# Performance work log

Hardware: AMD Instinct MI355X
Metric: run time of the kernel (lower is better)

The kernel has to match this reference:

```python
import jax, jax.numpy as jnp
import numpy as np

B, S, H = 32, 128, 768
MH, MT = 6, 8            # max holder / target span sizes
M = max(MH, MT)          # max span size -> M conv widths (1..M)
KH, KT = 4, 4            # max n holders / targets per sentence


def _forward(embedding, mask, wh, bh, wt, bt, wi, bi, we, be):
    Bz, Sz, Hz = embedding.shape
    # --- multi-scale span averaging (Conv1d with identity box filters == moving mean) ---
    cs = jnp.concatenate([jnp.zeros((Bz, 1, Hz), embedding.dtype),
                          jnp.cumsum(embedding, axis=1)], axis=1)  # [B,S+1,H]
    reps = [embedding]
    for w in range(2, M + 1):
        mean = (cs[:, w:, :] - cs[:, :-w, :]) / float(w)          # [B,S-w+1,H]
        reps.append(jnp.pad(mean, ((0, 0), (0, w - 1), (0, 0))))  # zero-pad tail like torch.cat
    span = jnp.concatenate(reps, axis=1)                          # [B, M*S, H]; index = S*width_idx + start
    # --- span validity masks (span must fit within sentence length) ---
    lengths = jnp.sum(mask, axis=1)                               # [B]
    pos = jnp.arange(Sz)
    widths = jnp.arange(M)
    base = pos[None, None, :] < (lengths[:, None, None] - widths[None, :, None])  # [B,M,S]
    holder_valid = (base & (widths[None, :, None] < MH)).reshape(Bz, M * Sz)
    target_valid = (base & (widths[None, :, None] < MT)).reshape(Bz, M * Sz)
    # --- span scoring (sigmoid linear), invalid spans forced to -1 ---
    hs = jnp.where(holder_valid, jax.nn.sigmoid(span @ wh + bh), -1.0)  # [B, M*S]
    ts = jnp.where(target_valid, jax.nn.sigmoid(span @ wt + bt), -1.0)
    # --- top-k span selection (== argsort descending, take first K) ---
    vt, it = jax.lax.top_k(ts, KT)
    vh, ih = jax.lax.top_k(hs, KH)
    tval = vt > 0.0                                                # [B,KT]
    hval = vh > 0.0                                                # [B,KH]
    trep = jnp.take_along_axis(span, it[:, :, None], axis=1)      # [B,KT,H]
    hrep = jnp.take_along_axis(span, ih[:, :, None], axis=1)      # [B,KH,H]
    implicit_input = trep * tval[:, :, None].astype(span.dtype)   # zeros where invalid
    pair_valid = (hval[:, :, None] & tval[:, None, :])            # [B,KH,KT]
    pair = jnp.concatenate([jnp.broadcast_to(hrep[:, :, None, :], (Bz, KH, KT, Hz)),
                            jnp.broadcast_to(trep[:, None, :, :], (Bz, KH, KT, Hz))], axis=-1)
    explicit_input = (pair * pair_valid[..., None].astype(span.dtype)).reshape(Bz, KH * KT, 2 * Hz)
    implicit_logits = implicit_input @ wi + bi                    # [B,KT,4]
    explicit_logits = explicit_input @ we + be                    # [B,KH*KT,4]
    return implicit_logits, explicit_logits, hs, ts


def setup_inputs() -> dict:
    key = jax.random.key(0)
    ks = jax.random.split(key, 8)
    embedding = jax.random.normal(ks[0], (B, S, H), jnp.float32)
    mask = jax.random.randint(ks[1], (B, S), 0, 2).astype(jnp.int32)
    wh = jax.random.normal(ks[2], (H,), jnp.float32) * 0.02
    bh = jnp.zeros((), jnp.float32)
    wt = jax.random.normal(ks[3], (H,), jnp.float32) * 0.02
    bt = jnp.zeros((), jnp.float32)
    wi = jax.random.normal(ks[4], (H, 4), jnp.float32) * 0.02
    bi = jnp.zeros((4,), jnp.float32)
    we = jax.random.normal(ks[5], (2 * H, 4), jnp.float32) * 0.02
    be = jnp.zeros((4,), jnp.float32)
    return dict(embedding=embedding, mask=mask, wh=wh, bh=bh, wt=wt, bt=bt,
                wi=wi, bi=bi, we=we, be=be)


def reference(embedding, mask, wh, bh, wt, bt, wi, bi, we, be):
    return _forward(embedding, mask, wh, bh, wt, bt, wi, bi, we, be)
```

## Files before the change

### kernel.cpp

```cpp
#include <hip/hip_runtime.h>

namespace {
constexpr int Bsz = 32;
constexpr int Ssz = 128;
constexpr int Hsz = 768;
constexpr int Msz = 8;
constexpr int MHs = 6;
constexpr int NSPAN = Msz * Ssz;
}

__device__ __forceinline__ bool gtpair(float av, int ai, float bv, int bi) {
    return (av > bv) || (av == bv && ai < bi);
}

struct Top4 { float v[4]; int ix[4]; };

__device__ __forceinline__ void t4_init(Top4& t) {
#pragma unroll
    for (int k = 0; k < 4; ++k) { t.v[k] = -3.f; t.ix[k] = 0x7fffffff; }
}

__device__ __forceinline__ void t4_insert_g(Top4& a, float cv, int ci) {
    bool g0 = gtpair(cv, ci, a.v[0], a.ix[0]);
    bool g1 = gtpair(cv, ci, a.v[1], a.ix[1]);
    bool g2 = gtpair(cv, ci, a.v[2], a.ix[2]);
    bool g3 = gtpair(cv, ci, a.v[3], a.ix[3]);
    float nv3 = g2 ? a.v[2]  : (g3 ? cv : a.v[3]);
    int   ni3 = g2 ? a.ix[2] : (g3 ? ci : a.ix[3]);
    float nv2 = g1 ? a.v[1]  : (g2 ? cv : a.v[2]);
    int   ni2 = g1 ? a.ix[1] : (g2 ? ci : a.ix[2]);
    float nv1 = g0 ? a.v[0]  : (g1 ? cv : a.v[1]);
    int   ni1 = g0 ? a.ix[0] : (g1 ? ci : a.ix[1]);
    float nv0 = g0 ? cv : a.v[0];
    int   ni0 = g0 ? ci : a.ix[0];
    a.v[0] = nv0; a.ix[0] = ni0;
    a.v[1] = nv1; a.ix[1] = ni1;
    a.v[2] = nv2; a.ix[2] = ni2;
    a.v[3] = nv3; a.ix[3] = ni3;
}

__device__ __forceinline__ void t4_merge_into(Top4& a, const Top4& b) {
#pragma unroll
    for (int k = 0; k < 4; ++k) t4_insert_g(a, b.v[k], b.ix[k]);
}

__device__ __forceinline__ Top4 t4_wave_merge(Top4 t) {
#pragma unroll
    for (int off = 1; off < 64; off <<= 1) {
        Top4 o;
#pragma unroll
        for (int k = 0; k < 4; ++k) {
            o.v[k]  = __shfl_xor(t.v[k], off);
            o.ix[k] = __shfl_xor(t.ix[k], off);
        }
        t4_merge_into(t, o);
    }
    return t;
}

__global__ __launch_bounds__(256) void row_dots_kernel(
    const float* __restrict__ emb, const float* __restrict__ wh,
    const float* __restrict__ wt, float* __restrict__ dh, float* __restrict__ dt)
{
    int wave = blockIdx.x * 4 + (threadIdx.x >> 6);
    int lane = threadIdx.x & 63;
    int row0 = wave * 2;

    const float4* wh4 = (const float4*)wh;
    const float4* wt4 = (const float4*)wt;
    float4 WH0 = wh4[lane], WH1 = wh4[lane + 64], WH2 = wh4[lane + 128];
    float4 WT0 = wt4[lane], WT1 = wt4[lane + 64], WT2 = wt4[lane + 128];

    const float4* r0 = (const float4*)(emb + (size_t)row0 * Hsz);
    const float4* r1 = r0 + (Hsz / 4);
    float4 a0 = r0[lane], a1 = r0[lane + 64], a2 = r0[lane + 128];
    float4 b0 = r1[lane], b1 = r1[lane + 64], b2 = r1[lane + 128];

    float ph0 = 0.f, pt0 = 0.f, ph1 = 0.f, pt1 = 0.f;
    ph0 = fmaf(a0.x, WH0.x, fmaf(a0.y, WH0.y, fmaf(a0.z, WH0.z, fmaf(a0.w, WH0.w, ph0))));
    ph0 = fmaf(a1.x, WH1.x, fmaf(a1.y, WH1.y, fmaf(a1.z, WH1.z, fmaf(a1.w, WH1.w, ph0))));
    ph0 = fmaf(a2.x, WH2.x, fmaf(a2.y, WH2.y, fmaf(a2.z, WH2.z, fmaf(a2.w, WH2.w, ph0))));
    pt0 = fmaf(a0.x, WT0.x, fmaf(a0.y, WT0.y, fmaf(a0.z, WT0.z, fmaf(a0.w, WT0.w, pt0))));
    pt0 = fmaf(a1.x, WT1.x, fmaf(a1.y, WT1.y, fmaf(a1.z, WT1.z, fmaf(a1.w, WT1.w, pt0))));
    pt0 = fmaf(a2.x, WT2.x, fmaf(a2.y, WT2.y, fmaf(a2.z, WT2.z, fmaf(a2.w, WT2.w, pt0))));
    ph1 = fmaf(b0.x, WH0.x, fmaf(b0.y, WH0.y, fmaf(b0.z, WH0.z, fmaf(b0.w, WH0.w, ph1))));
    ph1 = fmaf(b1.x, WH1.x, fmaf(b1.y, WH1.y, fmaf(b1.z, WH1.z, fmaf(b1.w, WH1.w, ph1))));
    ph1 = fmaf(b2.x, WH2.x, fmaf(b2.y, WH2.y, fmaf(b2.z, WH2.z, fmaf(b2.w, WH2.w, ph1))));
    pt1 = fmaf(b0.x, WT0.x, fmaf(b0.y, WT0.y, fmaf(b0.z, WT0.z, fmaf(b0.w, WT0.w, pt1))));
    pt1 = fmaf(b1.x, WT1.x, fmaf(b1.y, WT1.y, fmaf(b1.z, WT1.z, fmaf(b1.w, WT1.w, pt1))));
    pt1 = fmaf(b2.x, WT2.x, fmaf(b2.y, WT2.y, fmaf(b2.z, WT2.z, fmaf(b2.w, WT2.w, pt1))));

#pragma unroll
    for (int off = 32; off; off >>= 1) {
        ph0 += __shfl_down(ph0, off);
        pt0 += __shfl_down(pt0, off);
        ph1 += __shfl_down(ph1, off);
        pt1 += __shfl_down(pt1, off);
    }
    if (lane == 0) {
        dh[row0] = ph0; dt[row0] = pt0;
        dh[row0 + 1] = ph1; dt[row0 + 1] = pt1;
    }
}

__global__ __launch_bounds__(256) void per_batch_kernel(
    const float* __restrict__ emb, const int* __restrict__ mask,
    const float* __restrict__ bh_p, const float* __restrict__ bt_p,
    const float* __restrict__ wi, const float* __restrict__ bi,
    const float* __restrict__ we, const float* __restrict__ be,
    const float* __restrict__ dh, const float* __restrict__ dt,
    float* __restrict__ out)
{
    const int b = blockIdx.x;
    const int tid = threadIdx.x;
    const int wavei = tid >> 6, lane = tid & 63;

    __shared__ float dsh[Ssz], dst_[Ssz];
    __shared__ int   len_s;
    __shared__ float swv[4][4];
    __shared__ int   swi[4][4];
    __shared__ int   sel[8];
    __shared__ int   val[8];
    __shared__ float proj[8][8];

    if (tid < Ssz) {
        dsh[tid]  = dh[b * Ssz + tid];
        dst_[tid] = dt[b * Ssz + tid];
    }
    if (wavei == 0) {
        int m = mask[b * Ssz + lane] + mask[b * Ssz + lane + 64];
#pragma unroll
        for (int off = 32; off; off >>= 1) m += __shfl_down(m, off);
        if (lane == 0) len_s = m;
    }
    __syncthreads();

    const int   len = len_s;
    const float bhv = bh_p[0], btv = bt_p[0];
    float* out_impl = out;
    float* out_expl = out + Bsz * 16;
    float* out_hs   = out_expl + Bsz * 64;
    float* out_ts   = out_hs + Bsz * NSPAN;

    {
        const int st  = tid & (Ssz - 1);
        const int grp = tid >> 7;
        const float* dar = grp ? dsh : dst_;
        const float  bv  = grp ? bhv : btv;
        float* outp = grp ? (out_hs + b * NSPAN) : (out_ts + b * NSPAN);
        Top4 t4l; t4_init(t4l);
        float run = 0.f;
#pragma unroll
        for (int widx = 0; widx < Msz; ++widx) {
            bool fits = (st < len - widx);
            if (fits) run += dar[st + widx];
            bool valid = fits && (grp == 0 || widx < MHs);
            float sc = -1.f;
            if (valid) {
                float x = run * (1.f / (float)(widx + 1)) + bv;
                sc = 1.f / (1.f + __expf(-x));
            }
            int i = (widx << 7) | st;
            outp[i] = sc;
            t4_insert_g(t4l, sc, i);
        }
        t4l = t4_wave_merge(t4l);
        if (lane == 0) {
#pragma unroll
            for (int k = 0; k < 4; ++k) { swv[wavei][k] = t4l.v[k]; swi[wavei][k] = t4l.ix[k]; }
        }
    }
    __syncthreads();

    if (tid < 2) {
        Top4 a, c;
#pragma unroll
        for (int k = 0; k < 4; ++k) {
            a.v[k] = swv[2 * tid][k];     a.ix[k] = swi[2 * tid][k];
            c.v[k] = swv[2 * tid + 1][k]; c.ix[k] = swi[2 * tid + 1][k];
        }
        t4_merge_into(a, c);
#pragma unroll
        for (int k = 0; k < 4; ++k) {
            sel[tid * 4 + k] = a.ix[k];
            val[tid * 4 + k] = (a.v[k] > 0.f) ? 1 : 0;
        }
    }
    __syncthreads();

    for (int s2 = 0; s2 < 2; ++s2) {
        int slot = wavei + 4 * s2;
        float acc[8] = {0.f, 0.f, 0.f, 0.f, 0.f, 0.f, 0.f, 0.f};
        if (val[slot]) {
            int idx = sel[slot];
            int w = (idx >> 7) + 1, st = idx & (Ssz - 1);
            const float4* base = (const float4*)(emb + ((size_t)b * Ssz + st) * Hsz);
            float inv = 1.f / (float)w;
            float4 s0 = {0,0,0,0}, s1 = {0,0,0,0}, s2v = {0,0,0,0};
#pragma unroll
            for (int r = 0; r < Msz; ++r) {
                int   rr = (r < w) ? r : (w - 1);
                float m_ = (r < w) ? inv : 0.f;
                const float4* rp = base + rr * (Hsz / 4);
                float4 e0 = rp[lane];
                float4 e1 = rp[lane + 64];
                float4 e2 = rp[lane + 128];
                s0.x = fmaf(e0.x, m_, s0.x); s0.y = fmaf(e0.y, m_, s0.y);
                s0.z = fmaf(e0.z, m_, s0.z); s0.w = fmaf(e0.w, m_, s0.w);
                s1.x = fmaf(e1.x, m_, s1.x); s1.y = fmaf(e1.y, m_, s1.y);
                s1.z = fmaf(e1.z, m_, s1.z); s1.w = fmaf(e1.w, m_, s1.w);
                s2v.x = fmaf(e2.x, m_, s2v.x); s2v.y = fmaf(e2.y, m_, s2v.y);
                s2v.z = fmaf(e2.z, m_, s2v.z); s2v.w = fmaf(e2.w, m_, s2v.w);
            }
            const float4* wi4 = (const float4*)wi;
            const float4* we4 = (const float4*)we;
#pragma unroll
            for (int ii = 0; ii < 3; ++ii) {
                float4 rep = (ii == 0) ? s0 : ((ii == 1) ? s1 : s2v);
                float reps[4] = {rep.x, rep.y, rep.z, rep.w};
                int j = lane + 64 * ii;
                if (s2 == 0) {
#pragma unroll
                    for (int t = 0; t < 4; ++t) {
                        float rt = reps[t];
                        float4 a = wi4[4 * j + t];
                        float4 c = we4[Hsz + 4 * j + t];
                        acc[0] = fmaf(rt, a.x, acc[0]); acc[1] = fmaf(rt, a.y, acc[1]);
                        acc[2] = fmaf(rt, a.z, acc[2]); acc[3] = fmaf(rt, a.w, acc[3]);
                        acc[4] = fmaf(rt, c.x, acc[4]); acc[5] = fmaf(rt, c.y, acc[5]);
                        acc[6] = fmaf(rt, c.z, acc[6]); acc[7] = fmaf(rt, c.w, acc[7]);
                    }
                } else {
#pragma unroll
                    for (int t = 0; t < 4; ++t) {
                        float rt = reps[t];
                        float4 c = we4[4 * j + t];
                        acc[0] = fmaf(rt, c.x, acc[0]); acc[1] = fmaf(rt, c.y, acc[1]);
                        acc[2] = fmaf(rt, c.z, acc[2]); acc[3] = fmaf(rt, c.w, acc[3]);
                    }
                }
            }
        }
#pragma unroll
        for (int off = 32; off; off >>= 1)
#pragma unroll
            for (int c = 0; c < 8; ++c) acc[c] += __shfl_down(acc[c], off);
        if (lane == 0)
#pragma unroll
            for (int c = 0; c < 8; ++c) proj[slot][c] = acc[c];
    }
    __syncthreads();

    if (tid < 16) {
        int k = tid >> 2, c = tid & 3;
        out_impl[b * 16 + tid] = bi[c] + (val[k] ? proj[k][c] : 0.f);
    } else if (tid >= 64 && tid < 128) {
        int u = tid - 64;
        int j = u >> 4, k = (u >> 2) & 3, c = u & 3;
        float v = be[c];
        if (val[4 + j] && val[k]) v += proj[4 + j][c] + proj[k][4 + c];
        out_expl[b * 64 + u] = v;
    }
}

extern "C" void kernel_launch(void* const* d_in, const int* in_sizes, int n_in,
                              void* d_out, int out_size, void* d_ws, size_t ws_size,
                              hipStream_t stream) {
    const float* emb  = (const float*)d_in[0];
    const int*   mask = (const int*)d_in[1];
    const float* wh   = (const float*)d_in[2];
    const float* bh   = (const float*)d_in[3];
    const float* wt   = (const float*)d_in[4];
    const float* bt   = (const float*)d_in[5];
    const float* wi   = (const float*)d_in[6];
    const float* bi   = (const float*)d_in[7];
    const float* we   = (const float*)d_in[8];
    const float* be   = (const float*)d_in[9];
    float* out = (float*)d_out;

    float* dh = (float*)d_ws;
    float* dt = dh + Bsz * Ssz;

    row_dots_kernel<<<512, 256, 0, stream>>>(emb, wh, wt, dh, dt);
    per_batch_kernel<<<Bsz, 256, 0, stream>>>(emb, mask, bh, bt, wi, bi, we, be,
                                              dh, dt, out);
}
```

Baseline: 92.43 us.

## Prefetch projection weights into padded LDS and merge target/holder gather passes

```diff
diff --git a/kernel.cpp b/kernel.cpp
--- a/kernel.cpp
+++ b/kernel.cpp
@@ -122,6 +122,8 @@
     __shared__ int   sel[8];
     __shared__ int   val[8];
     __shared__ float proj[8][8];
+    __shared__ float4 wi_s[(Hsz / 4) * 5];
+    __shared__ float4 we_s[(2 * Hsz / 4) * 5];
 
     if (tid < Ssz) {
         dsh[tid]  = dh[b * Ssz + tid];
@@ -134,6 +136,18 @@
         if (lane == 0) len_s = m;
     }
     __syncthreads();
+
+    const float4* wi4g = (const float4*)wi;
+    const float4* we4g = (const float4*)we;
+    float4 wreg0 = wi4g[tid];
+    float4 wreg1 = wi4g[tid + 256];
+    float4 wreg2 = wi4g[tid + 512];
+    float4 wreg3 = we4g[tid];
+    float4 wreg4 = we4g[tid + 256];
+    float4 wreg5 = we4g[tid + 512];
+    float4 wreg6 = we4g[tid + 768];
+    float4 wreg7 = we4g[tid + 1024];
+    float4 wreg8 = we4g[tid + 1280];
 
     const int   len = len_s;
     const float bhv = bh_p[0], btv = bt_p[0];
@@ -170,6 +184,27 @@
             for (int k = 0; k < 4; ++k) { swv[wavei][k] = t4l.v[k]; swi[wavei][k] = t4l.ix[k]; }
         }
     }
+
+    {
+        int i0 = tid;
+        wi_s[5 * (i0 >> 2) + (i0 & 3)] = wreg0;
+        int i1 = tid + 256;
+        wi_s[5 * (i1 >> 2) + (i1 & 3)] = wreg1;
+        int i2 = tid + 512;
+        wi_s[5 * (i2 >> 2) + (i2 & 3)] = wreg2;
+        int j0 = tid;
+        we_s[5 * (j0 >> 2) + (j0 & 3)] = wreg3;
+        int j1 = tid + 256;
+        we_s[5 * (j1 >> 2) + (j1 & 3)] = wreg4;
+        int j2 = tid + 512;
+        we_s[5 * (j2 >> 2) + (j2 & 3)] = wreg5;
+        int j3 = tid + 768;
+        we_s[5 * (j3 >> 2) + (j3 & 3)] = wreg6;
+        int j4 = tid + 1024;
+        we_s[5 * (j4 >> 2) + (j4 & 3)] = wreg7;
+        int j5 = tid + 1280;
+        we_s[5 * (j5 >> 2) + (j5 & 3)] = wreg8;
+    }
     __syncthreads();
 
     if (tid < 2) {
@@ -188,66 +223,79 @@
     }
     __syncthreads();
 
-    for (int s2 = 0; s2 < 2; ++s2) {
-        int slot = wavei + 4 * s2;
-        float acc[8] = {0.f, 0.f, 0.f, 0.f, 0.f, 0.f, 0.f, 0.f};
-        if (val[slot]) {
-            int idx = sel[slot];
-            int w = (idx >> 7) + 1, st = idx & (Ssz - 1);
-            const float4* base = (const float4*)(emb + ((size_t)b * Ssz + st) * Hsz);
-            float inv = 1.f / (float)w;
-            float4 s0 = {0,0,0,0}, s1 = {0,0,0,0}, s2v = {0,0,0,0};
-#pragma unroll
-            for (int r = 0; r < Msz; ++r) {
-                int   rr = (r < w) ? r : (w - 1);
-                float m_ = (r < w) ? inv : 0.f;
-                const float4* rp = base + rr * (Hsz / 4);
-                float4 e0 = rp[lane];
-                float4 e1 = rp[lane + 64];
-                float4 e2 = rp[lane + 128];
-                s0.x = fmaf(e0.x, m_, s0.x); s0.y = fmaf(e0.y, m_, s0.y);
-                s0.z = fmaf(e0.z, m_, s0.z); s0.w = fmaf(e0.w, m_, s0.w);
-                s1.x = fmaf(e1.x, m_, s1.x); s1.y = fmaf(e1.y, m_, s1.y);
-                s1.z = fmaf(e1.z, m_, s1.z); s1.w = fmaf(e1.w, m_, s1.w);
-                s2v.x = fmaf(e2.x, m_, s2v.x); s2v.y = fmaf(e2.y, m_, s2v.y);
-                s2v.z = fmaf(e2.z, m_, s2v.z); s2v.w = fmaf(e2.w, m_, s2v.w);
+    {
+        const int tIdx = sel[wavei],    hIdx = sel[wavei + 4];
+        const int tvld = val[wavei],    hvld = val[wavei + 4];
+        const int tw = (tIdx >> 7) + 1, tst = tIdx & (Ssz - 1);
+        const int hw = (hIdx >> 7) + 1, hst = hIdx & (Ssz - 1);
+        const int   gtw  = tvld ? tw : 1;
+        const int   gtst = tvld ? tst : 0;
+        const int   ghw  = hvld ? hw : 1;
+        const int   ghst = hvld ? hst : 0;
+        const float tinv = tvld ? (1.f / (float)tw) : 0.f;
+        const float hinv = hvld ? (1.f / (float)hw) : 0.f;
+        const float4* tbase = (const float4*)(emb + ((size_t)b * Ssz + gtst) * Hsz);
+        const float4* hbase = (const float4*)(emb + ((size_t)b * Ssz + ghst) * Hsz);
+
+        float4 t0 = {0,0,0,0}, t1 = {0,0,0,0}, t2 = {0,0,0,0};
+        float4 h0 = {0,0,0,0}, h1 = {0,0,0,0}, h2 = {0,0,0,0};
+#pragma unroll
+        for (int r = 0; r < Msz; ++r) {
+            int   trr = (r < gtw) ? r : (gtw - 1);
+            float tm  = (r < gtw) ? tinv : 0.f;
+            int   hrr = (r < ghw) ? r : (ghw - 1);
+            float hm  = (r < ghw) ? hinv : 0.f;
+            const float4* trp = tbase + trr * (Hsz / 4);
+            const float4* hrp = hbase + hrr * (Hsz / 4);
+            float4 a0 = trp[lane], a1 = trp[lane + 64], a2 = trp[lane + 128];
+            float4 c0 = hrp[lane], c1 = hrp[lane + 64], c2 = hrp[lane + 128];
+            t0.x = fmaf(a0.x, tm, t0.x); t0.y = fmaf(a0.y, tm, t0.y);
+            t0.z = fmaf(a0.z, tm, t0.z); t0.w = fmaf(a0.w, tm, t0.w);
+            t1.x = fmaf(a1.x, tm, t1.x); t1.y = fmaf(a1.y, tm, t1.y);
+            t1.z = fmaf(a1.z, tm, t1.z); t1.w = fmaf(a1.w, tm, t1.w);
+            t2.x = fmaf(a2.x, tm, t2.x); t2.y = fmaf(a2.y, tm, t2.y);
+            t2.z = fmaf(a2.z, tm, t2.z); t2.w = fmaf(a2.w, tm, t2.w);
+            h0.x = fmaf(c0.x, hm, h0.x); h0.y = fmaf(c0.y, hm, h0.y);
+            h0.z = fmaf(c0.z, hm, h0.z); h0.w = fmaf(c0.w, hm, h0.w);
+            h1.x = fmaf(c1.x, hm, h1.x); h1.y = fmaf(c1.y, hm, h1.y);
+            h1.z = fmaf(c1.z, hm, h1.z); h1.w = fmaf(c1.w, hm, h1.w);
+            h2.x = fmaf(c2.x, hm, h2.x); h2.y = fmaf(c2.y, hm, h2.y);
+            h2.z = fmaf(c2.z, hm, h2.z); h2.w = fmaf(c2.w, hm, h2.w);
+        }
+
+        float acc[12] = {0,0,0,0,0,0,0,0,0,0,0,0};
+#pragma unroll
+        for (int ii = 0; ii < 3; ++ii) {
+            float4 trep = (ii == 0) ? t0 : ((ii == 1) ? t1 : t2);
+            float4 hrep = (ii == 0) ? h0 : ((ii == 1) ? h1 : h2);
+            float tr[4] = {trep.x, trep.y, trep.z, trep.w};
+            float hr[4] = {hrep.x, hrep.y, hrep.z, hrep.w};
+            int j = lane + 64 * ii;
+#pragma unroll
+            for (int t = 0; t < 4; ++t) {
+                float4 a  = wi_s[5 * j + t];
+                float4 cb = we_s[5 * (j + Hsz / 4) + t];
+                float4 ct = we_s[5 * j + t];
+                float rt = tr[t], rh = hr[t];
+                acc[0] = fmaf(rt, a.x,  acc[0]); acc[1] = fmaf(rt, a.y,  acc[1]);
+                acc[2] = fmaf(rt, a.z,  acc[2]); acc[3] = fmaf(rt, a.w,  acc[3]);
+                acc[4] = fmaf(rt, cb.x, acc[4]); acc[5] = fmaf(rt, cb.y, acc[5]);
+                acc[6] = fmaf(rt, cb.z, acc[6]); acc[7] = fmaf(rt, cb.w, acc[7]);
+                acc[8]  = fmaf(rh, ct.x, acc[8]);  acc[9]  = fmaf(rh, ct.y, acc[9]);
+                acc[10] = fmaf(rh, ct.z, acc[10]); acc[11] = fmaf(rh, ct.w, acc[11]);
             }
-            const float4* wi4 = (const float4*)wi;
-            const float4* we4 = (const float4*)we;
-#pragma unroll
-            for (int ii = 0; ii < 3; ++ii) {
-                float4 rep = (ii == 0) ? s0 : ((ii == 1) ? s1 : s2v);
-                float reps[4] = {rep.x, rep.y, rep.z, rep.w};
-                int j = lane + 64 * ii;
-                if (s2 == 0) {
-#pragma unroll
-                    for (int t = 0; t < 4; ++t) {
-                        float rt = reps[t];
-                        float4 a = wi4[4 * j + t];
-                        float4 c = we4[Hsz + 4 * j + t];
-                        acc[0] = fmaf(rt, a.x, acc[0]); acc[1] = fmaf(rt, a.y, acc[1]);
-                        acc[2] = fmaf(rt, a.z, acc[2]); acc[3] = fmaf(rt, a.w, acc[3]);
-                        acc[4] = fmaf(rt, c.x, acc[4]); acc[5] = fmaf(rt, c.y, acc[5]);
-                        acc[6] = fmaf(rt, c.z, acc[6]); acc[7] = fmaf(rt, c.w, acc[7]);
-                    }
-                } else {
-#pragma unroll
-                    for (int t = 0; t < 4; ++t) {
-                        float rt = reps[t];
-                        float4 c = we4[4 * j + t];
-                        acc[0] = fmaf(rt, c.x, acc[0]); acc[1] = fmaf(rt, c.y, acc[1]);
-                        acc[2] = fmaf(rt, c.z, acc[2]); acc[3] = fmaf(rt, c.w, acc[3]);
-                    }
-                }
-            }
-        }
+        }
+
 #pragma unroll
         for (int off = 32; off; off >>= 1)
 #pragma unroll
-            for (int c = 0; c < 8; ++c) acc[c] += __shfl_down(acc[c], off);
-        if (lane == 0)
-#pragma unroll
-            for (int c = 0; c < 8; ++c) proj[slot][c] = acc[c];
+            for (int c = 0; c < 12; ++c) acc[c] += __shfl_down(acc[c], off);
+        if (lane == 0) {
+#pragma unroll
+            for (int c = 0; c < 8; ++c) proj[wavei][c] = acc[c];
+#pragma unroll
+            for (int c = 0; c < 4; ++c) proj[wavei + 4][c] = acc[8 + c];
+        }
     }
     __syncthreads();
 
```

Result: no change. 91.13 us (-1.4%).
